# Optimization experiments

Hardware: AMD Instinct MI355X
Metric: run time of the kernel (lower is better)

The kernel has to match this reference:

```python
import jax, jax.numpy as jnp
import numpy as np

# Straight-through-estimator round (round_pass in the original code)
def _round_ste(x):
    return x + jax.lax.stop_gradient(jnp.round(x) - x)

INPUT_QMAX = 127.0   # 2**(input_bit-1)-1,  input_bit=8
WEIGHT_QMAX = 127.0  # 2**(weight_bit-1)-1, weight_bit=8
OUT_RANGE = 127.0    # 2**(output_bit-1)-1, output_bit=8


def setup_inputs() -> dict:
    key = jax.random.key(0)
    k0, k1, k2 = jax.random.split(key, 3)
    B, Cin, Cout, H, W, K = 16, 320, 320, 64, 64, 3
    x = jax.random.normal(k0, (B, Cin, H, W), dtype=jnp.float32)
    weight = jax.random.normal(k1, (Cout, Cin, K, K), dtype=jnp.float32) * 0.05
    bias = jax.random.normal(k2, (Cout,), dtype=jnp.float32) * 0.1
    # LSQ learned scalar step sizes (cloned from conv_lsq in the original)
    step_x = jnp.float32(0.02)
    step_w = jnp.float32(0.002)
    step_b = jnp.float32(0.01)
    # Bit_shift_layer scale: shift conv accumulator down into output_bit range
    shift_scale = jnp.float32(2.0 ** -7)
    return {"x": x, "weight": weight, "bias": bias, "step_x": step_x,
            "step_w": step_w, "step_b": step_b, "shift_scale": shift_scale}


def reference(x, weight, bias, step_x, step_w, step_b, shift_scale):
    # --- lsq_quant_input (isint=True): x_int in [-127,127], x_scale = 1/step ---
    x_int = jnp.clip(_round_ste(x / step_x), -INPUT_QMAX, INPUT_QMAX)
    x_scale = 1.0 / step_x
    # --- lsq_quant_weight (isint=True) ---
    w_int = jnp.clip(_round_ste(weight / step_w), -WEIGHT_QMAX, WEIGHT_QMAX)
    w_scale = 1.0 / step_w
    # --- Conv2d_int: integer-valued conv (no bias) ---
    y_int = jax.lax.conv_general_dilated(
        x_int, w_int, window_strides=(1, 1), padding=((1, 1), (1, 1)),
        dimension_numbers=("NCHW", "OIHW", "NCHW"))
    # --- mvm_result_shift: bit-shift accumulator into output range ---
    y_shift = jnp.clip(_round_ste(y_int * shift_scale), -OUT_RANGE, OUT_RANGE)
    # --- lsq_quant_bias (isint=False): dequantized bias ---
    b_deq = jnp.clip(_round_ste(bias / step_b), -OUT_RANGE, OUT_RANGE) * step_b
    # --- bias requant to output int scale, add, clamp (fused epilogue) ---
    b_int8 = jnp.clip(_round_ste(b_deq * shift_scale * x_scale * w_scale),
                      -OUT_RANGE, OUT_RANGE)
    y_shift_dmac = jnp.clip(y_shift + b_int8[None, :, None, None],
                            -OUT_RANGE, OUT_RANGE)
    # module returns y_shift_DMAC (the integer-valued clamped output)
    return y_shift_dmac
```

## Files before the change

### kernel.cpp

```cpp
#include <hip/hip_runtime.h>

typedef int v4i __attribute__((ext_vector_type(4)));

#define QMAX 127.0f

#define XQ_BYTES 22302720
#define WQ_BYTES 921600

__device__ __forceinline__ float clampf(float v, float lo, float hi) {
    return fminf(fmaxf(v, lo), hi);
}

__device__ __forceinline__ float qround(float v, float step, float inv) {
    float t = v * inv;
    float r = rintf(t);
    float d = fabsf(t - r);
    if (fabsf(d - 0.5f) < fabsf(t) * 1e-5f + 1e-5f)
        r = rintf(v / step);
    return r;
}

__device__ __forceinline__ void gload_lds16(const char* g, char* l) {
    __builtin_amdgcn_global_load_lds(
        (const __attribute__((address_space(1))) void*)g,
        (__attribute__((address_space(3))) void*)l, 16, 0, 0);
}

__device__ __forceinline__ v4i mfma_i8(v4i a, v4i b, v4i c) {
    return __builtin_amdgcn_mfma_i32_16x16x64_i8(a, b, c, 0, 0, 0);
}

__global__ __launch_bounds__(256) void quant_x_kernel(
    const float* __restrict__ x, const float* __restrict__ step_p,
    char* __restrict__ xq)
{
    __shared__ float F[64 * 65];
    const int t = threadIdx.x;
    const int h = blockIdx.x;
    const int b = blockIdx.y;
    const float step = *step_p;
    const float inv  = 1.0f / step;
    const int w  = t >> 2;
    const int cg = t & 3;
    v4i vals[5];

    for (int c5 = 0; c5 < 5; ++c5) {
        {
            const int r = t >> 4, c = (t & 15) * 4;
            const float* src = x + (((size_t)(b * 320 + c5 * 64) * 64 + h) * 64);
#pragma unroll
            for (int i = 0; i < 4; ++i) {
                const int row = r + i * 16;
                *(float4*)&F[row * 65 + c] =
                    *(const float4*)(src + (size_t)row * 4096 + c);
            }
        }
        __syncthreads();
        int dws[4];
#pragma unroll
        for (int j = 0; j < 4; ++j) {
            int word = 0;
#pragma unroll
            for (int k = 0; k < 4; ++k) {
                float v = F[(cg * 16 + j * 4 + k) * 65 + w];
                int xi = (int)clampf(qround(v, step, inv), -QMAX, QMAX);
                word |= (xi & 0xFF) << (8 * k);
            }
            dws[j] = word;
        }
        vals[c5] = (v4i){dws[0], dws[1], dws[2], dws[3]};
        __syncthreads();
    }

    const int col = w + 1;
    const int key = (col >> 1) & 3;
    char* base = xq + ((size_t)(b * 66 + (h + 1)) * 66 + col) * 320;
#pragma unroll
    for (int c5 = 0; c5 < 5; ++c5)
        *(v4i*)(base + c5 * 64 + (((cg ^ key)) << 4)) = vals[c5];
}

__global__ __launch_bounds__(256) void prep_kernel(
    const float* __restrict__ w, const float* __restrict__ bias,
    const float* __restrict__ step_w_p, const float* __restrict__ step_b_p,
    const float* __restrict__ step_x_p, const float* __restrict__ shift_p,
    char* __restrict__ wq2, char* __restrict__ xq, float* __restrict__ bi)
{
    const int bid = blockIdx.x;
    if (bid < 3600) {
        const int tid = bid * 256 + threadIdx.x;
        const float step = *step_w_p;
        const float inv  = 1.0f / step;
        const int p    = tid / 102400;
        const int r    = tid - p * 102400;
        const int c5   = r / 20480;
        const int r2   = r - c5 * 20480;
        const int cog  = r2 >> 10;
        const int r3   = r2 & 1023;
        const int lane = r3 >> 4, j = r3 & 15;
        const int co = cog * 16 + (lane & 15);
        const int ci = c5 * 64 + (lane >> 4) * 16 + j;
        float v = w[(size_t)co * 2880 + ci * 9 + p];
        int q = (int)clampf(qround(v, step, inv), -QMAX, QMAX);
        wq2[tid] = (char)q;
    } else if (bid < 3925) {
        int tid = (bid - 3600) * 256 + threadIdx.x;
        if (tid < 83200) {
            int b = tid / 5200;
            int r = tid - b * 5200;
            int px = r / 20;
            int ck = (r - px * 20) * 16;
            int row, col;
            if (px < 66)       { row = 0;  col = px; }
            else if (px < 132) { row = 65; col = px - 66; }
            else { int e = px - 132; row = 1 + (e >> 1); col = (e & 1) * 65; }
            size_t off = ((size_t)(b * 66 + row) * 66 + col) * 320 + ck;
            v4i z = {0, 0, 0, 0};
            *(v4i*)&xq[off] = z;
        }
    } else {
        const float step_b = *step_b_p;
        const float xs = 1.0f / *step_x_p;
        const float ws = 1.0f / *step_w_p;
        const float shift = *shift_p;
#pragma unroll
        for (int co = threadIdx.x; co < 320; co += 256) {
            float b_deq = clampf(rintf(bias[co] / step_b), -QMAX, QMAX) * step_b;
            float v = ((b_deq * shift) * xs) * ws;
            bi[co] = clampf(rintf(v), -QMAX, QMAX);
        }
    }
}

__global__ __launch_bounds__(256, 3) void conv_mfma_kernel(
    const char* __restrict__ xq, const char* __restrict__ wq2,
    const float* __restrict__ bi, const float* __restrict__ shift_p,
    float* __restrict__ out)
{
    __shared__ __attribute__((aligned(16))) char B_lds[2][25344];

    const int t   = threadIdx.x;
    const int bx  = blockIdx.x;
    const int co0 = bx * 64;
    const int ptile = blockIdx.y;
    const int b  = ptile >> 4;
    const int h0 = (ptile & 15) * 4;

    const int wave = t >> 6, lane = t & 63;
    const int quad = lane >> 4, l15 = lane & 15;

    const char* xbase = xq + ((size_t)(b * 66 + h0) * 66) * 320;

    int bcol[3][4];
#pragma unroll
    for (int dw = 0; dw < 3; ++dw)
#pragma unroll
        for (int i = 0; i < 4; ++i) {
            const int col = i * 16 + l15 + dw;
            const int key = (col >> 1) & 3;
            bcol[dw][i] = col * 64 + ((quad ^ key) << 4);
        }

    v4i acc[4][4] = {};

    for (int c = t; c < 1584; c += 256) {
        const char* g = xbase + (c >> 2) * 320 + ((c & 3) << 4);
        gload_lds16(g, &B_lds[0][(c - lane) * 16]);
    }
    __syncthreads();

    for (int c5 = 0; c5 < 5; ++c5) {
        const char* Bw = &B_lds[c5 & 1][wave * 4224];
        const char* wp = wq2 + (c5 * 20 + bx * 4) * 1024 + lane * 16;

        v4i a[2][4], bf[2][4];
#pragma unroll
        for (int cs = 0; cs < 4; ++cs)
            a[0][cs] = *(const v4i*)(wp + cs * 1024);
#pragma unroll
        for (int i = 0; i < 4; ++i)
            bf[0][i] = *(const v4i*)(Bw + bcol[0][i]);

#pragma unroll
        for (int p = 0; p < 9; ++p) {
            const int cur = p & 1, nxt = cur ^ 1;
            if (p < 8) {
                const int pn = p + 1;
                const int dh1 = pn / 3, dw1 = pn - dh1 * 3;
#pragma unroll
                for (int cs = 0; cs < 4; ++cs)
                    a[nxt][cs] = *(const v4i*)(wp + pn * 102400 + cs * 1024);
#pragma unroll
                for (int i = 0; i < 4; ++i)
                    bf[nxt][i] = *(const v4i*)(Bw + dh1 * 4224 + bcol[dw1][i]);
            }
            if (p == 1 && c5 < 4) {
                const int ci0 = (c5 + 1) * 64;
                char* dst = B_lds[(c5 + 1) & 1];
                for (int c = t; c < 1584; c += 256) {
                    const char* g = xbase + (c >> 2) * 320 + ci0 + ((c & 3) << 4);
                    gload_lds16(g, &dst[(c - lane) * 16]);
                }
            }
#pragma unroll
            for (int i = 0; i < 4; ++i)
#pragma unroll
                for (int cs = 0; cs < 4; ++cs)
                    acc[cs][i] = mfma_i8(a[cur][cs], bf[cur][i], acc[cs][i]);
        }
        __syncthreads();
    }

    const float shift = *shift_p;
    const int h = h0 + wave;
#pragma unroll
    for (int cs = 0; cs < 4; ++cs) {
#pragma unroll
        for (int reg = 0; reg < 4; ++reg) {
            const int co = co0 + cs * 16 + quad * 4 + reg;
            const float bv = bi[co];
            float* orow = out + (((size_t)(b * 320 + co) * 64) + h) * 64;
#pragma unroll
            for (int i = 0; i < 4; ++i) {
                float y  = (float)acc[cs][i][reg];
                float ys = clampf(rintf(y * shift), -QMAX, QMAX);
                orow[i * 16 + l15] = clampf(ys + bv, -QMAX, QMAX);
            }
        }
    }
}

extern "C" void kernel_launch(void* const* d_in, const int* in_sizes, int n_in,
                              void* d_out, int out_size, void* d_ws, size_t ws_size,
                              hipStream_t stream) {
    const float* x      = (const float*)d_in[0];
    const float* w      = (const float*)d_in[1];
    const float* bias   = (const float*)d_in[2];
    const float* step_x = (const float*)d_in[3];
    const float* step_w = (const float*)d_in[4];
    const float* step_b = (const float*)d_in[5];
    const float* shift  = (const float*)d_in[6];
    float* out = (float*)d_out;

    char*  xq  = (char*)d_ws;
    char*  wq2 = xq + XQ_BYTES;
    float* bi  = (float*)(wq2 + WQ_BYTES);

    quant_x_kernel<<<dim3(64, 16), 256, 0, stream>>>(x, step_x, xq);
    prep_kernel<<<3926, 256, 0, stream>>>(w, bias, step_w, step_b, step_x, shift,
                                          wq2, xq, bi);
    conv_mfma_kernel<<<dim3(5, 256), 256, 0, stream>>>(xq, wq2, bi, shift, out);
}
```

Before: 226.0 us.

## Give each wave a private LDS input slab and drop block barriers

```diff
diff --git a/kernel.cpp b/kernel.cpp
--- a/kernel.cpp
+++ b/kernel.cpp
@@ -132,12 +132,14 @@
     }
 }
 
+#define SLAB 13312
+
 __global__ __launch_bounds__(256, 3) void conv_mfma_kernel(
     const char* __restrict__ xq, const char* __restrict__ wq2,
     const float* __restrict__ bi, const float* __restrict__ shift_p,
     float* __restrict__ out)
 {
-    __shared__ __attribute__((aligned(16))) char B_lds[2][25344];
+    __shared__ __attribute__((aligned(16))) char B_lds[4 * SLAB];
 
     const int t   = threadIdx.x;
     const int bx  = blockIdx.x;
@@ -149,7 +151,8 @@
     const int wave = t >> 6, lane = t & 63;
     const int quad = lane >> 4, l15 = lane & 15;
 
-    const char* xbase = xq + ((size_t)(b * 66 + h0) * 66) * 320;
+    const char* xw = xq + ((size_t)(b * 66 + h0 + wave) * 66) * 320;
+    char* slab = &B_lds[wave * SLAB];
 
     int bcol[3][4];
 #pragma unroll
@@ -163,14 +166,20 @@
 
     v4i acc[4][4] = {};
 
-    for (int c = t; c < 1584; c += 256) {
-        const char* g = xbase + (c >> 2) * 320 + ((c & 3) << 4);
-        gload_lds16(g, &B_lds[0][(c - lane) * 16]);
-    }
-    __syncthreads();
+    {
+#pragma unroll
+        for (int i = 0; i < 12; ++i) {
+            const int c = i * 64 + lane;
+            gload_lds16(xw + (c >> 2) * 320 + ((c & 3) << 4), slab + i * 1024);
+        }
+        const int c = 768 + lane;
+        if (lane < 24)
+            gload_lds16(xw + (c >> 2) * 320 + ((c & 3) << 4), slab + 12 * 1024);
+    }
 
     for (int c5 = 0; c5 < 5; ++c5) {
-        const char* Bw = &B_lds[c5 & 1][wave * 4224];
+        __builtin_amdgcn_s_waitcnt(0x0F70);
+
         const char* wp = wq2 + (c5 * 20 + bx * 4) * 1024 + lane * 16;
 
         v4i a[2][4], bf[2][4];
@@ -179,7 +188,7 @@
             a[0][cs] = *(const v4i*)(wp + cs * 1024);
 #pragma unroll
         for (int i = 0; i < 4; ++i)
-            bf[0][i] = *(const v4i*)(Bw + bcol[0][i]);
+            bf[0][i] = *(const v4i*)(slab + bcol[0][i]);
 
 #pragma unroll
         for (int p = 0; p < 9; ++p) {
@@ -192,15 +201,21 @@
                     a[nxt][cs] = *(const v4i*)(wp + pn * 102400 + cs * 1024);
 #pragma unroll
                 for (int i = 0; i < 4; ++i)
-                    bf[nxt][i] = *(const v4i*)(Bw + dh1 * 4224 + bcol[dw1][i]);
-            }
-            if (p == 1 && c5 < 4) {
+                    bf[nxt][i] = *(const v4i*)(slab + dh1 * 4224 + bcol[dw1][i]);
+            }
+            if (p == 8 && c5 < 4) {
+                __builtin_amdgcn_s_waitcnt(0xC07F);
                 const int ci0 = (c5 + 1) * 64;
-                char* dst = B_lds[(c5 + 1) & 1];
-                for (int c = t; c < 1584; c += 256) {
-                    const char* g = xbase + (c >> 2) * 320 + ci0 + ((c & 3) << 4);
-                    gload_lds16(g, &dst[(c - lane) * 16]);
+#pragma unroll
+                for (int i = 0; i < 12; ++i) {
+                    const int c = i * 64 + lane;
+                    gload_lds16(xw + (c >> 2) * 320 + ci0 + ((c & 3) << 4),
+                                slab + i * 1024);
                 }
+                const int c = 768 + lane;
+                if (lane < 24)
+                    gload_lds16(xw + (c >> 2) * 320 + ci0 + ((c & 3) << 4),
+                                slab + 12 * 1024);
             }
 #pragma unroll
             for (int i = 0; i < 4; ++i)
@@ -208,7 +223,6 @@
                 for (int cs = 0; cs < 4; ++cs)
                     acc[cs][i] = mfma_i8(a[cur][cs], bf[cur][i], acc[cs][i]);
         }
-        __syncthreads();
     }
 
     const float shift = *shift_p;
```

New measurement: 231.3 us. +2.3%, slower.
